# Optimization experiments

Hardware: AMD Instinct MI355X
Metric: run time of the kernel (lower is better)

The kernel has to match this reference:

```python
import jax, jax.numpy as jnp
import numpy as np

N, M, E = 50000, 50000, 1600000
D_IN, HID, OUT = 128, 128, 128


def setup_inputs() -> dict:
    key = jax.random.key(0)
    ks = jax.random.split(key, 8)
    query = jax.random.normal(ks[0], (N, D_IN), jnp.float32)
    memory = jax.random.normal(ks[1], (M, D_IN), jnp.float32)
    adj_vals = jnp.ones((E,), jnp.float32)  # tf.sparse adjacency values (typically 1.0)
    Wq = jax.random.normal(ks[2], (D_IN, HID), jnp.float32) * 0.05
    bq = jnp.zeros((HID,), jnp.float32)
    Wk = jax.random.normal(ks[3], (D_IN, HID), jnp.float32) * 0.05
    bk = jnp.zeros((HID,), jnp.float32)
    Wv = jax.random.normal(ks[4], (D_IN, OUT), jnp.float32) * 0.05
    bv = jnp.zeros((OUT,), jnp.float32)
    rows = jnp.sort(jax.random.randint(ks[5], (E,), 0, N, jnp.int32))
    cols = jax.random.randint(ks[6], (E,), 0, M, jnp.int32)
    return {"query": query, "memory": memory, "adj_vals": adj_vals,
            "Wq": Wq, "bq": bq, "Wk": Wk, "bk": bk, "Wv": Wv, "bv": bv,
            "rows": rows, "cols": cols}


def reference(query, memory, adj_vals, Wq, bq, Wk, bk, Wv, bv, rows, cols):
    n = query.shape[0]
    hid = Wq.shape[1]
    # Dense projections with gelu (tfa.activations.gelu default approximate=True)
    q = jax.nn.gelu(query @ Wq + bq, approximate=True)   # [n, hid]
    k = jax.nn.gelu(memory @ Wk + bk, approximate=True)  # [m, hid]
    v = jax.nn.gelu(memory @ Wv + bv, approximate=True)  # [m, out]
    # Edge-level scores = (q_i . k_j) / sqrt(hid) * adj_val  (== coef * adj_matrix)
    scores = jnp.sum(q[rows] * k[cols], axis=-1)          # [E]
    scores = scores * (adj_vals / jnp.sqrt(jnp.float32(hid)))
    # Sparse softmax over nonzero entries of each row (tf.sparse.softmax)
    row_max = jax.ops.segment_max(scores, rows, num_segments=n, indices_are_sorted=True)
    row_max = jnp.where(jnp.isfinite(row_max), row_max, 0.0)  # rows with no edges
    e = jnp.exp(scores - row_max[rows])
    denom = jax.ops.segment_sum(e, rows, num_segments=n, indices_are_sorted=True)
    w = e / denom[rows]                                   # [E]
    # Sparse-dense matmul: out_i = sum_j w_ij * v_j
    out = jax.ops.segment_sum(w[:, None] * v[cols], rows, num_segments=n, indices_are_sorted=True)
    return out
```

## Files before the change

### kernel.cpp

```cpp
#include <hip/hip_runtime.h>
#include <hip/hip_bf16.h>
#include <math.h>

typedef __bf16 bf16x8 __attribute__((ext_vector_type(8)));
typedef float f32x4 __attribute__((ext_vector_type(4)));

#define DIM 128

__global__ __launch_bounds__(256) void prep_w_kernel(
    const float* __restrict__ Wq, const float* __restrict__ Wk,
    const float* __restrict__ Wv, __bf16* __restrict__ Wt)
{
    const float* W = (blockIdx.y == 0) ? Wq : (blockIdx.y == 1) ? Wk : Wv;
    __bf16* dst = Wt + (size_t)blockIdx.y * DIM * DIM;
    int idx = blockIdx.x * 256 + threadIdx.x;
    int k = idx >> 7;
    int n = idx & 127;
    dst[n * DIM + k] = (__bf16)W[idx];
}

__global__ __launch_bounds__(256) void row_ptr_kernel(
    const int* __restrict__ rows, int* __restrict__ row_ptr, int n, int e)
{
    int r = blockIdx.x * 256 + threadIdx.x;
    if (r > n) return;
    if (r == n) { row_ptr[n] = e; return; }
    int lo = 0, hi = e;
    while (lo < hi) {
        int mid = (lo + hi) >> 1;
        if (rows[mid] < r) lo = mid + 1; else hi = mid;
    }
    row_ptr[r] = lo;
}

__global__ __launch_bounds__(256) void proj_gemm_kernel(
    const float* __restrict__ query, const float* __restrict__ memory,
    const __bf16* __restrict__ Wt,
    const float* __restrict__ bq, const float* __restrict__ bk,
    const float* __restrict__ bv,
    __bf16* __restrict__ qout, __bf16* __restrict__ kout,
    __bf16* __restrict__ vout, int n, int m)
{
    int which = blockIdx.y;
    const float* X    = (which == 0) ? query : memory;
    const __bf16* Wm  = Wt + (size_t)which * DIM * DIM;
    const float* bias = (which == 0) ? bq : (which == 1) ? bk : bv;
    __bf16* Y         = (which == 0) ? qout : (which == 1) ? kout : vout;
    int R             = (which == 0) ? n : m;

    int wave = threadIdx.x >> 6;
    int lane = threadIdx.x & 63;
    int quad = lane >> 4;
    int l16  = lane & 15;
    int row_base = blockIdx.x * 128 + wave * 32;
    if (row_base >= R) return;

    bf16x8 afrag[2][4];
    for (int rt = 0; rt < 2; ++rt) {
        int row = row_base + rt * 16 + l16;
        if (row >= R) row = R - 1;
        const float* xp = X + (size_t)row * DIM + quad * 8;
        for (int ks = 0; ks < 4; ++ks) {
            float4 x0 = *(const float4*)(xp + ks * 32);
            float4 x1 = *(const float4*)(xp + ks * 32 + 4);
            bf16x8 a;
            a[0] = (__bf16)x0.x; a[1] = (__bf16)x0.y;
            a[2] = (__bf16)x0.z; a[3] = (__bf16)x0.w;
            a[4] = (__bf16)x1.x; a[5] = (__bf16)x1.y;
            a[6] = (__bf16)x1.z; a[7] = (__bf16)x1.w;
            afrag[rt][ks] = a;
        }
    }

    for (int ct = 0; ct < 8; ++ct) {
        const __bf16* wp = Wm + (size_t)(ct * 16 + l16) * DIM + quad * 8;
        f32x4 acc0 = {0.f, 0.f, 0.f, 0.f};
        f32x4 acc1 = {0.f, 0.f, 0.f, 0.f};
        for (int ks = 0; ks < 4; ++ks) {
            bf16x8 b = *(const bf16x8*)(wp + ks * 32);
            acc0 = __builtin_amdgcn_mfma_f32_16x16x32_bf16(afrag[0][ks], b, acc0, 0, 0, 0);
            acc1 = __builtin_amdgcn_mfma_f32_16x16x32_bf16(afrag[1][ks], b, acc1, 0, 0, 0);
        }
        float bval = bias[ct * 16 + l16];
        for (int rt = 0; rt < 2; ++rt) {
            f32x4 acc = rt ? acc1 : acc0;
            for (int reg = 0; reg < 4; ++reg) {
                int row = row_base + rt * 16 + quad * 4 + reg;
                if (row < R) {
                    float x = acc[reg] + bval;
                    float t  = 0.7978845608028654f * (x + 0.044715f * x * x * x);
                    float th = 1.0f - 2.0f / (__expf(2.0f * t) + 1.0f);
                    float g  = 0.5f * x * (1.0f + th);
                    Y[(size_t)row * DIM + ct * 16 + l16] = (__bf16)g;
                }
            }
        }
    }
}

__global__ __launch_bounds__(256) void edge_attn_kernel(
    const __bf16* __restrict__ qmat, const __bf16* __restrict__ kmat,
    const __bf16* __restrict__ vmat, const float* __restrict__ adj_vals,
    const int* __restrict__ cols, const int* __restrict__ row_ptr,
    float* __restrict__ out, int n)
{
    int row = blockIdx.x * 4 + (threadIdx.x >> 6);
    if (row >= n) return;
    int lane    = threadIdx.x & 63;
    int quarter = lane >> 4;
    int l16     = lane & 15;

    int start = row_ptr[row];
    int end   = row_ptr[row + 1];

    float qv[8];
    {
        bf16x8 qb = *(const bf16x8*)(qmat + (size_t)row * DIM + l16 * 8);
        for (int j = 0; j < 8; ++j) qv[j] = (float)qb[j];
    }

    float m_q = -1e30f, s_q = 0.0f;
    float acc[8];
    for (int j = 0; j < 8; ++j) acc[j] = 0.0f;

    const float inv_sqrt_d = 0.08838834764831845f;

    int ng = (end - start + 3) >> 2;
    for (int g = 0; g < ng; ++g) {
        int e = start + g * 4 + quarter;
        bool valid = (e < end);
        int   col = valid ? cols[e]     : 0;
        float adj = valid ? adj_vals[e] : 0.0f;
        bf16x8 kb = *(const bf16x8*)(kmat + (size_t)col * DIM + l16 * 8);
        bf16x8 vb = *(const bf16x8*)(vmat + (size_t)col * DIM + l16 * 8);
        float partial = 0.0f;
        for (int j = 0; j < 8; ++j) partial += qv[j] * (float)kb[j];
        partial += __shfl_xor(partial, 1);
        partial += __shfl_xor(partial, 2);
        partial += __shfl_xor(partial, 4);
        partial += __shfl_xor(partial, 8);
        float score = valid ? partial * adj * inv_sqrt_d : -1e30f;
        float m_new = fmaxf(m_q, score);
        float f = __expf(m_q - m_new);
        float p = valid ? __expf(score - m_new) : 0.0f;
        s_q = s_q * f + p;
        m_q = m_new;
        for (int j = 0; j < 8; ++j) acc[j] = acc[j] * f + p * (float)vb[j];
    }

    float m_all = m_q;
    m_all = fmaxf(m_all, __shfl_xor(m_all, 16));
    m_all = fmaxf(m_all, __shfl_xor(m_all, 32));
    float f = __expf(m_q - m_all);
    float s_sc = s_q * f;
    s_sc += __shfl_xor(s_sc, 16);
    s_sc += __shfl_xor(s_sc, 32);
    float inv = (s_sc > 0.0f) ? 1.0f / s_sc : 0.0f;

    float o[8];
    for (int j = 0; j < 8; ++j) {
        float a = acc[j] * f;
        a += __shfl_xor(a, 16);
        a += __shfl_xor(a, 32);
        o[j] = a * inv;
    }
    if (quarter == 0) {
        float4* dst = (float4*)(out + (size_t)row * DIM + l16 * 8);
        dst[0] = make_float4(o[0], o[1], o[2], o[3]);
        dst[1] = make_float4(o[4], o[5], o[6], o[7]);
    }
}

extern "C" void kernel_launch(void* const* d_in, const int* in_sizes, int n_in,
                              void* d_out, int out_size, void* d_ws, size_t ws_size,
                              hipStream_t stream)
{
    const float* query    = (const float*)d_in[0];
    const float* memory   = (const float*)d_in[1];
    const float* adj_vals = (const float*)d_in[2];
    const float* Wq       = (const float*)d_in[3];
    const float* bq       = (const float*)d_in[4];
    const float* Wk       = (const float*)d_in[5];
    const float* bk       = (const float*)d_in[6];
    const float* Wv       = (const float*)d_in[7];
    const float* bv       = (const float*)d_in[8];
    const int*   rows     = (const int*)d_in[9];
    const int*   cols     = (const int*)d_in[10];
    float* out = (float*)d_out;

    int n = in_sizes[0] / DIM;
    int m = in_sizes[1] / DIM;
    int e = in_sizes[9];

    char* ws = (char*)d_ws;
    size_t off = 0;
    __bf16* Wt = (__bf16*)(ws + off); off += (size_t)3 * DIM * DIM * 2;
    __bf16* qb = (__bf16*)(ws + off); off += (size_t)n * DIM * 2;
    __bf16* kb = (__bf16*)(ws + off); off += (size_t)m * DIM * 2;
    __bf16* vb = (__bf16*)(ws + off); off += (size_t)m * DIM * 2;
    int* row_ptr = (int*)(ws + off);  off += (size_t)(n + 1) * 4;

    prep_w_kernel<<<dim3(64, 3), 256, 0, stream>>>(Wq, Wk, Wv, Wt);

    row_ptr_kernel<<<dim3((n + 1 + 255) / 256), 256, 0, stream>>>(rows, row_ptr, n, e);

    int max_r = (n > m) ? n : m;
    proj_gemm_kernel<<<dim3((max_r + 127) / 128, 3), 256, 0, stream>>>(
        query, memory, Wt, bq, bk, bv, qb, kb, vb, n, m);

    edge_attn_kernel<<<dim3((n + 3) / 4), 256, 0, stream>>>(
        qb, kb, vb, adj_vals, cols, row_ptr, out, n);
}
```

Measured before the change: 261.2 us.

## Interleave K/V rows, stage GEMM through LDS, switch to fp16, unroll edge loop

```diff
diff --git a/kernel.cpp b/kernel.cpp
--- a/kernel.cpp
+++ b/kernel.cpp
@@ -2,21 +2,23 @@
 #include <hip/hip_bf16.h>
 #include <math.h>
 
-typedef __bf16 bf16x8 __attribute__((ext_vector_type(8)));
+typedef _Float16 f16x4 __attribute__((ext_vector_type(4)));
+typedef _Float16 f16x8 __attribute__((ext_vector_type(8)));
 typedef float f32x4 __attribute__((ext_vector_type(4)));
 
 #define DIM 128
+#define LDST 136
 
 __global__ __launch_bounds__(256) void prep_w_kernel(
     const float* __restrict__ Wq, const float* __restrict__ Wk,
-    const float* __restrict__ Wv, __bf16* __restrict__ Wt)
+    const float* __restrict__ Wv, _Float16* __restrict__ Wt)
 {
     const float* W = (blockIdx.y == 0) ? Wq : (blockIdx.y == 1) ? Wk : Wv;
-    __bf16* dst = Wt + (size_t)blockIdx.y * DIM * DIM;
+    _Float16* dst = Wt + (size_t)blockIdx.y * DIM * DIM;
     int idx = blockIdx.x * 256 + threadIdx.x;
     int k = idx >> 7;
     int n = idx & 127;
-    dst[n * DIM + k] = (__bf16)W[idx];
+    dst[n * DIM + k] = (_Float16)W[idx];
 }
 
 __global__ __launch_bounds__(256) void row_ptr_kernel(
@@ -33,76 +35,94 @@
     row_ptr[r] = lo;
 }
 
-__global__ __launch_bounds__(256) void proj_gemm_kernel(
+__global__ __launch_bounds__(256, 2) void proj_gemm_kernel(
     const float* __restrict__ query, const float* __restrict__ memory,
-    const __bf16* __restrict__ Wt,
+    const _Float16* __restrict__ Wt,
     const float* __restrict__ bq, const float* __restrict__ bk,
     const float* __restrict__ bv,
-    __bf16* __restrict__ qout, __bf16* __restrict__ kout,
-    __bf16* __restrict__ vout, int n, int m)
-{
+    _Float16* __restrict__ qf, _Float16* __restrict__ kv, int n, int m)
+{
+    __shared__ _Float16 xs[128 * LDST];
+
     int which = blockIdx.y;
     const float* X    = (which == 0) ? query : memory;
-    const __bf16* Wm  = Wt + (size_t)which * DIM * DIM;
+    const _Float16* Wm = Wt + (size_t)which * DIM * DIM;
     const float* bias = (which == 0) ? bq : (which == 1) ? bk : bv;
-    __bf16* Y         = (which == 0) ? qout : (which == 1) ? kout : vout;
     int R             = (which == 0) ? n : m;
-
-    int wave = threadIdx.x >> 6;
-    int lane = threadIdx.x & 63;
+    _Float16* Ybase   = (which == 0) ? qf : (which == 2) ? kv + DIM : kv;
+    size_t Ystride    = (which == 0) ? DIM : 2 * DIM;
+
+    int tid = threadIdx.x;
+    int rowblock = blockIdx.x * 128;
+    if (rowblock >= R) return;
+
+    for (int it = 0; it < 16; ++it) {
+        int flat = it * 256 + tid;
+        int r  = flat >> 5;
+        int c4 = (flat & 31) * 4;
+        int gr = rowblock + r;
+        if (gr >= R) gr = R - 1;
+        float4 x = *(const float4*)(X + (size_t)gr * DIM + c4);
+        f16x4 w4;
+        w4[0] = (_Float16)x.x; w4[1] = (_Float16)x.y;
+        w4[2] = (_Float16)x.z; w4[3] = (_Float16)x.w;
+        *(f16x4*)(&xs[r * LDST + c4]) = w4;
+    }
+    __syncthreads();
+
+    int wave = tid >> 6;
+    int lane = tid & 63;
     int quad = lane >> 4;
     int l16  = lane & 15;
-    int row_base = blockIdx.x * 128 + wave * 32;
-    if (row_base >= R) return;
-
-    bf16x8 afrag[2][4];
-    for (int rt = 0; rt < 2; ++rt) {
-        int row = row_base + rt * 16 + l16;
-        if (row >= R) row = R - 1;
-        const float* xp = X + (size_t)row * DIM + quad * 8;
+    int wrow = wave * 32;
+
+    f16x8 afrag[2][4];
+    for (int rt = 0; rt < 2; ++rt)
+        for (int ks = 0; ks < 4; ++ks)
+            afrag[rt][ks] = *(const f16x8*)(&xs[(wrow + rt * 16 + l16) * LDST + quad * 8 + ks * 32]);
+
+    f32x4 acc[8][2];
+    for (int ct = 0; ct < 8; ++ct) { acc[ct][0] = {0,0,0,0}; acc[ct][1] = {0,0,0,0}; }
+    for (int ct = 0; ct < 8; ++ct) {
+        const _Float16* wp = Wm + (size_t)(ct * 16 + l16) * DIM + quad * 8;
         for (int ks = 0; ks < 4; ++ks) {
-            float4 x0 = *(const float4*)(xp + ks * 32);
-            float4 x1 = *(const float4*)(xp + ks * 32 + 4);
-            bf16x8 a;
-            a[0] = (__bf16)x0.x; a[1] = (__bf16)x0.y;
-            a[2] = (__bf16)x0.z; a[3] = (__bf16)x0.w;
-            a[4] = (__bf16)x1.x; a[5] = (__bf16)x1.y;
-            a[6] = (__bf16)x1.z; a[7] = (__bf16)x1.w;
-            afrag[rt][ks] = a;
+            f16x8 b = *(const f16x8*)(wp + ks * 32);
+            acc[ct][0] = __builtin_amdgcn_mfma_f32_16x16x32_f16(afrag[0][ks], b, acc[ct][0], 0, 0, 0);
+            acc[ct][1] = __builtin_amdgcn_mfma_f32_16x16x32_f16(afrag[1][ks], b, acc[ct][1], 0, 0, 0);
         }
     }
 
+    __syncthreads();
     for (int ct = 0; ct < 8; ++ct) {
-        const __bf16* wp = Wm + (size_t)(ct * 16 + l16) * DIM + quad * 8;
-        f32x4 acc0 = {0.f, 0.f, 0.f, 0.f};
-        f32x4 acc1 = {0.f, 0.f, 0.f, 0.f};
-        for (int ks = 0; ks < 4; ++ks) {
-            bf16x8 b = *(const bf16x8*)(wp + ks * 32);
-            acc0 = __builtin_amdgcn_mfma_f32_16x16x32_bf16(afrag[0][ks], b, acc0, 0, 0, 0);
-            acc1 = __builtin_amdgcn_mfma_f32_16x16x32_bf16(afrag[1][ks], b, acc1, 0, 0, 0);
-        }
         float bval = bias[ct * 16 + l16];
         for (int rt = 0; rt < 2; ++rt) {
-            f32x4 acc = rt ? acc1 : acc0;
             for (int reg = 0; reg < 4; ++reg) {
-                int row = row_base + rt * 16 + quad * 4 + reg;
-                if (row < R) {
-                    float x = acc[reg] + bval;
-                    float t  = 0.7978845608028654f * (x + 0.044715f * x * x * x);
-                    float th = 1.0f - 2.0f / (__expf(2.0f * t) + 1.0f);
-                    float g  = 0.5f * x * (1.0f + th);
-                    Y[(size_t)row * DIM + ct * 16 + l16] = (__bf16)g;
-                }
+                float x = acc[ct][rt][reg] + bval;
+                float t  = 0.7978845608028654f * (x + 0.044715f * x * x * x);
+                float th = 1.0f - 2.0f / (__expf(2.0f * t) + 1.0f);
+                float g  = 0.5f * x * (1.0f + th);
+                xs[(wrow + rt * 16 + quad * 4 + reg) * LDST + ct * 16 + l16] = (_Float16)g;
             }
         }
     }
+    __syncthreads();
+
+    for (int it = 0; it < 8; ++it) {
+        int flat = it * 256 + tid;
+        int r  = flat >> 4;
+        int c8 = (flat & 15) * 8;
+        int gr = rowblock + r;
+        if (gr < R) {
+            f16x8 vv = *(const f16x8*)(&xs[r * LDST + c8]);
+            *(f16x8*)(Ybase + (size_t)gr * Ystride + c8) = vv;
+        }
+    }
 }
 
 __global__ __launch_bounds__(256) void edge_attn_kernel(
-    const __bf16* __restrict__ qmat, const __bf16* __restrict__ kmat,
-    const __bf16* __restrict__ vmat, const float* __restrict__ adj_vals,
-    const int* __restrict__ cols, const int* __restrict__ row_ptr,
-    float* __restrict__ out, int n)
+    const _Float16* __restrict__ qf, const _Float16* __restrict__ kv,
+    const float* __restrict__ adj_vals, const int* __restrict__ cols,
+    const int* __restrict__ row_ptr, float* __restrict__ out, int n)
 {
     int row = blockIdx.x * 4 + (threadIdx.x >> 6);
     if (row >= n) return;
@@ -115,7 +135,7 @@
 
     float qv[8];
     {
-        bf16x8 qb = *(const bf16x8*)(qmat + (size_t)row * DIM + l16 * 8);
+        f16x8 qb = *(const f16x8*)(qf + (size_t)row * DIM + l16 * 8);
         for (int j = 0; j < 8; ++j) qv[j] = (float)qb[j];
     }
 
@@ -123,29 +143,41 @@
     float acc[8];
     for (int j = 0; j < 8; ++j) acc[j] = 0.0f;
 
-    const float inv_sqrt_d = 0.08838834764831845f;
-
-    int ng = (end - start + 3) >> 2;
-    for (int g = 0; g < ng; ++g) {
-        int e = start + g * 4 + quarter;
-        bool valid = (e < end);
-        int   col = valid ? cols[e]     : 0;
-        float adj = valid ? adj_vals[e] : 0.0f;
-        bf16x8 kb = *(const bf16x8*)(kmat + (size_t)col * DIM + l16 * 8);
-        bf16x8 vb = *(const bf16x8*)(vmat + (size_t)col * DIM + l16 * 8);
-        float partial = 0.0f;
-        for (int j = 0; j < 8; ++j) partial += qv[j] * (float)kb[j];
-        partial += __shfl_xor(partial, 1);
-        partial += __shfl_xor(partial, 2);
-        partial += __shfl_xor(partial, 4);
-        partial += __shfl_xor(partial, 8);
-        float score = valid ? partial * adj * inv_sqrt_d : -1e30f;
-        float m_new = fmaxf(m_q, score);
-        float f = __expf(m_q - m_new);
-        float p = valid ? __expf(score - m_new) : 0.0f;
-        s_q = s_q * f + p;
+    const float scale = 0.08838834764831845f;
+
+    for (int g = start; g < end; g += 8) {
+        int eA = g + quarter;
+        int eB = g + 4 + quarter;
+        bool vA = eA < end;
+        bool vB = eB < end;
+        int   cA = vA ? cols[eA]     : 0;
+        int   cB = vB ? cols[eB]     : 0;
+        float aA = vA ? adj_vals[eA] : 0.0f;
+        float aB = vB ? adj_vals[eB] : 0.0f;
+        const _Float16* pA = kv + (size_t)cA * 256 + l16 * 8;
+        const _Float16* pB = kv + (size_t)cB * 256 + l16 * 8;
+        f16x8 kA = *(const f16x8*)pA;
+        f16x8 vA8 = *(const f16x8*)(pA + 128);
+        f16x8 kB = *(const f16x8*)pB;
+        f16x8 vB8 = *(const f16x8*)(pB + 128);
+
+        float dA = 0.0f, dB = 0.0f;
+        for (int j = 0; j < 8; ++j) { dA += qv[j] * (float)kA[j]; dB += qv[j] * (float)kB[j]; }
+        dA += __shfl_xor(dA, 1); dB += __shfl_xor(dB, 1);
+        dA += __shfl_xor(dA, 2); dB += __shfl_xor(dB, 2);
+        dA += __shfl_xor(dA, 4); dB += __shfl_xor(dB, 4);
+        dA += __shfl_xor(dA, 8); dB += __shfl_xor(dB, 8);
+
+        float sA = vA ? dA * aA * scale : -1e30f;
+        float sB = vB ? dB * aB * scale : -1e30f;
+        float m_new = fmaxf(m_q, fmaxf(sA, sB));
+        float f  = __expf(m_q - m_new);
+        float pA_ = vA ? __expf(sA - m_new) : 0.0f;
+        float pB_ = vB ? __expf(sB - m_new) : 0.0f;
+        s_q = s_q * f + pA_ + pB_;
         m_q = m_new;
-        for (int j = 0; j < 8; ++j) acc[j] = acc[j] * f + p * (float)vb[j];
+        for (int j = 0; j < 8; ++j)
+            acc[j] = acc[j] * f + pA_ * (float)vA8[j] + pB_ * (float)vB8[j];
     }
 
     float m_all = m_q;
@@ -194,20 +226,18 @@
 
     char* ws = (char*)d_ws;
     size_t off = 0;
-    __bf16* Wt = (__bf16*)(ws + off); off += (size_t)3 * DIM * DIM * 2;
-    __bf16* qb = (__bf16*)(ws + off); off += (size_t)n * DIM * 2;
-    __bf16* kb = (__bf16*)(ws + off); off += (size_t)m * DIM * 2;
-    __bf16* vb = (__bf16*)(ws + off); off += (size_t)m * DIM * 2;
-    int* row_ptr = (int*)(ws + off);  off += (size_t)(n + 1) * 4;
+    _Float16* Wt = (_Float16*)(ws + off); off += (size_t)3 * DIM * DIM * 2;
+    _Float16* qf = (_Float16*)(ws + off); off += (size_t)n * DIM * 2;
+    _Float16* kv = (_Float16*)(ws + off); off += (size_t)m * 2 * DIM * 2;
+    int* row_ptr = (int*)(ws + off);      off += (size_t)(n + 1) * 4;
 
     prep_w_kernel<<<dim3(64, 3), 256, 0, stream>>>(Wq, Wk, Wv, Wt);
 
     row_ptr_kernel<<<dim3((n + 1 + 255) / 256), 256, 0, stream>>>(rows, row_ptr, n, e);
 
-    int max_r = (n > m) ? n : m;
-    proj_gemm_kernel<<<dim3((max_r + 127) / 128, 3), 256, 0, stream>>>(
-        query, memory, Wt, bq, bk, bv, qb, kb, vb, n, m);
+    proj_gemm_kernel<<<dim3((n + 127) / 128, 3), 256, 0, stream>>>(
+        query, memory, Wt, bq, bk, bv, qf, kv, n, m);
 
     edge_attn_kernel<<<dim3((n + 3) / 4), 256, 0, stream>>>(
-        qb, kb, vb, adj_vals, cols, row_ptr, out, n);
-}
+        qf, kv, adj_vals, cols, row_ptr, out, n);
+}
```

New measurement: 261.4 us. Within noise of the previous version (+0.1%).
